# Kernel tuning notes

Hardware: AMD Instinct MI355X
Metric: run time of the kernel (lower is better)

Reference implementation:

```python
import jax, jax.numpy as jnp
import numpy as np

HID = 768
NUM_HEADS = 12
HEAD_DIM = HID // NUM_HEADS
MASK_VALUE = -1.0e9
EPS = 1.0e-4  # module's self.eps, also used as the diagonal fill constant


def setup_inputs() -> dict:
    key = jax.random.key(0)
    k1, k2, k3 = jax.random.split(key, 3)
    B, M = 16, 512
    ocr_features = jax.random.normal(k1, (B, M, HID), dtype=jnp.float32)
    # prior neighbor-attention from previous layer, probabilities in [0,1)
    prior = jax.random.uniform(k2, (B, 1, M, M), dtype=jnp.float32)
    Wq = jax.random.normal(k3, (HID, HID), dtype=jnp.float32) / np.sqrt(HID)
    bq = jnp.zeros((HID,), dtype=jnp.float32)
    ocr_features_mask = jnp.ones((B, M), dtype=jnp.int32)
    return {"ocr_features": ocr_features, "prior": prior, "Wq": Wq, "bq": bq,
            "ocr_features_mask": ocr_features_mask}


def reference(ocr_features, prior, Wq, bq, ocr_features_mask):
    B, M, _ = ocr_features.shape
    # Module uses q_linear for Q, K (and V, which is unused) -> Q == K.
    q = (ocr_features @ Wq + bq).reshape(B, M, NUM_HEADS, HEAD_DIM)
    q = q.transpose(0, 2, 1, 3)  # (B, H, M, D)
    # note: scaled by head_dim (not sqrt), as in the source
    scores = jnp.einsum('bhid,bhjd->bhij', q, q) / HEAD_DIM  # (B, H, M, M)

    dt = scores.dtype
    prev_word_mask = jnp.eye(M, k=1, dtype=dt)   # superdiagonal
    next_word_mask = jnp.eye(M, k=-1, dtype=dt)  # subdiagonal
    main_diag_mask = jnp.eye(M, dtype=dt)

    # neighbor mask: only prev/next word positions that are valid OCR tokens
    neibor_mask = ((prev_word_mask + next_word_mask)[None, :, :] > 0) & \
                  (ocr_features_mask[:, None, :] > 0)  # (B, M, M)
    scores = jnp.where(neibor_mask[:, None, :, :], scores, MASK_VALUE)
    neibor_attn = jax.nn.softmax(scores, axis=-1)
    # symmetrize: sqrt(a * a^T + eps)
    neibor_attn = jnp.sqrt(neibor_attn * jnp.swapaxes(neibor_attn, -1, -2) + EPS)
    neibor_attn = prior + (1.0 - prior) * neibor_attn

    # log-space cumulative product via triangular matmuls
    tri = jnp.triu(jnp.ones((M, M), dtype=dt))  # (M, M), incl. diagonal
    # keep only superdiagonal log-probs, cumulative-sum to the right via tri
    t = jnp.where(prev_word_mask > 0, jnp.log(neibor_attn + 1e-9), 0.0) @ tri
    g_attn = jnp.exp(jnp.einsum('ij,bhjk->bhik', tri, t))
    # zero out diagonal and lower triangle (tri - diag == 0 there)
    g_attn = jnp.where((tri - main_diag_mask) > 0, g_attn, 0.0)
    g_attn = g_attn + jnp.swapaxes(g_attn, -1, -2) + \
             jnp.where(main_diag_mask > 0, neibor_attn, EPS)
    return (g_attn, neibor_attn)
```

## Files before the change

### kernel.cpp

```cpp
#include <hip/hip_runtime.h>
#include <cstdint>
#include <cstddef>

#define B_   16
#define M_   512
#define HID_ 768
#define NH_  12
#define HD_  64

typedef short s16x8 __attribute__((ext_vector_type(8)));
typedef float f32x4 __attribute__((ext_vector_type(4)));
typedef unsigned short u16x8 __attribute__((ext_vector_type(8)));
typedef unsigned short u16x4 __attribute__((ext_vector_type(4)));

__device__ __forceinline__ unsigned short f2bf(float f) {
    unsigned int u = __builtin_bit_cast(unsigned int, f);
    u = u + 0x7FFFu + ((u >> 16) & 1u);
    return (unsigned short)(u >> 16);
}

__device__ __forceinline__ void gld_lds16(const void* g, void* lds) {
    __builtin_amdgcn_global_load_lds(
        (const __attribute__((address_space(1))) unsigned int*)g,
        (__attribute__((address_space(3))) unsigned int*)lds,
        16, 0, 0);
}

__launch_bounds__(256)
__global__ void prep(const float* __restrict__ X, const float* __restrict__ W,
                     unsigned short* __restrict__ Xb, unsigned short* __restrict__ Wt) {
    __shared__ float T[32][33];
    const int blk = blockIdx.x;
    const int t   = threadIdx.x;
    if (blk < 3072) {
        const size_t i = ((size_t)blk * 256 + t) * 8;
        const float4 a = *(const float4*)(X + i);
        const float4 b = *(const float4*)(X + i + 4);
        u16x8 v = { f2bf(a.x), f2bf(a.y), f2bf(a.z), f2bf(a.w),
                    f2bf(b.x), f2bf(b.y), f2bf(b.z), f2bf(b.w) };
        *(u16x8*)(Xb + i) = v;
    } else {
        const int tb = blk - 3072;
        const int n0 = (tb % 24) * 32;
        const int k0 = (tb / 24) * 32;
        #pragma unroll
        for (int p = 0; p < 4; ++p) {
            const int r = p * 8 + (t >> 5);
            const int c = t & 31;
            T[r][c] = W[(size_t)(k0 + r) * HID_ + n0 + c];
        }
        __syncthreads();
        const int nl = t >> 3;
        const int k4 = (t & 7) * 4;
        u16x4 v = { f2bf(T[k4 + 0][nl]), f2bf(T[k4 + 1][nl]),
                    f2bf(T[k4 + 2][nl]), f2bf(T[k4 + 3][nl]) };
        *(u16x4*)(Wt + (size_t)(n0 + nl) * HID_ + k0 + k4) = v;
    }
}

__launch_bounds__(256)
__global__ void gemm_qb(const unsigned short* __restrict__ Xb,
                        const unsigned short* __restrict__ Wt,
                        const float* __restrict__ bq, float* __restrict__ Q) {
    __shared__ unsigned short As[128 * 32];
    __shared__ unsigned short Bs[128 * 32];

    const int tid  = threadIdx.x;
    const int lane = tid & 63;
    const int wave = tid >> 6;
    const int wr   = (wave >> 1) * 64;
    const int wc   = (wave & 1) * 64;
    const int ln   = lane & 15;
    const int quad = lane >> 4;
    const int r0   = blockIdx.y * 128;
    const int n0   = blockIdx.x * 128;

    const int srow  = lane >> 2;
    const int skoff = (lane & 3) * 8;

    f32x4 acc[4][4] = {};

    for (int kt = 0; kt < HID_ / 32; ++kt) {
        const int k0 = kt * 32;
        #pragma unroll
        for (int c = wave * 2; c < wave * 2 + 2; ++c) {
            const unsigned short* ga = Xb + (size_t)(r0 + c * 16 + srow) * HID_ + k0 + skoff;
            gld_lds16(ga, (char*)As + c * 1024);
            const unsigned short* gb = Wt + (size_t)(n0 + c * 16 + srow) * HID_ + k0 + skoff;
            gld_lds16(gb, (char*)Bs + c * 1024);
        }
        __syncthreads();

        s16x8 af[4], bf[4];
        #pragma unroll
        for (int r = 0; r < 4; ++r)
            af[r] = *(const s16x8*)((const char*)As + (wr + r * 16 + ln) * 64 + quad * 16);
        #pragma unroll
        for (int c = 0; c < 4; ++c)
            bf[c] = *(const s16x8*)((const char*)Bs + (wc + c * 16 + ln) * 64 + quad * 16);
        #pragma unroll
        for (int r = 0; r < 4; ++r)
            #pragma unroll
            for (int c = 0; c < 4; ++c)
                acc[r][c] = __builtin_amdgcn_mfma_f32_16x16x32_bf16(af[r], bf[c], acc[r][c], 0, 0, 0);
        __syncthreads();
    }

    #pragma unroll
    for (int c = 0; c < 4; ++c) {
        const int col = n0 + wc + c * 16 + ln;
        const float bias = bq[col];
        #pragma unroll
        for (int r = 0; r < 4; ++r) {
            const int rowb = r0 + wr + r * 16 + quad * 4;
            #pragma unroll
            for (int e = 0; e < 4; ++e)
                Q[(size_t)(rowb + e) * HID_ + col] = acc[r][c][e] + bias;
        }
    }
}

__launch_bounds__(512)
__global__ void rowstats(const float* __restrict__ Q, const float* __restrict__ prior,
                         const int* __restrict__ mask,
                         float* __restrict__ na_super, float* __restrict__ na_sub,
                         float* __restrict__ Ssum) {
    const int bh = blockIdx.x;
    const int b  = bh / NH_;
    const int h  = bh - b * NH_;
    const int i  = threadIdx.x;
    const int lane = i & 63;
    const int wid  = i >> 6;

    __shared__ float sh_s[M_];
    __shared__ float sh_pp[M_];
    __shared__ float wsum[8];

    float s = 0.f;
    if (i < M_ - 1) {
        const float4* qa = (const float4*)(Q + (size_t)(b * M_ + i)     * HID_ + h * HD_);
        const float4* qb = (const float4*)(Q + (size_t)(b * M_ + i + 1) * HID_ + h * HD_);
        #pragma unroll
        for (int t = 0; t < 16; ++t) {
            float4 x = qa[t], y = qb[t];
            s += x.x * y.x + x.y * y.y + x.z * y.z + x.w * y.w;
        }
        s *= (1.f / 64.f);
    }
    sh_s[i] = s;
    __syncthreads();

    const bool vp = (i > 0)      && (mask[b * M_ + i - 1] > 0);
    const bool vn = (i < M_ - 1) && (mask[b * M_ + i + 1] > 0);
    const float sp = vp ? sh_s[i - 1] : -1e30f;
    const float sn = vn ? s : -1e30f;
    const float mx = fmaxf(sp, sn);
    const float ep = vp ? __expf(sp - mx) : 0.f;
    const float en = vn ? __expf(sn - mx) : 0.f;
    float den = ep + en;
    den = (den > 0.f) ? den : 1.f;
    const float pp = ep / den;
    const float pn = en / den;
    sh_pp[i] = pp;
    __syncthreads();

    float Lv = 0.f;
    if (i < M_ - 1) {
        const float  sym = sqrtf(pn * sh_pp[i + 1] + 1e-4f);
        const size_t pb  = (size_t)b * (M_ * M_);
        const float  prs = prior[pb + (size_t)i * M_ + (i + 1)];
        const float  prb = prior[pb + (size_t)(i + 1) * M_ + i];
        const float  nsup = prs + (1.f - prs) * sym;
        na_super[bh * M_ + i] = nsup;
        na_sub[bh * M_ + i]   = prb + (1.f - prb) * sym;
        Lv = logf(nsup + 1e-9f);
    }

    float v = Lv;
    #pragma unroll
    for (int off = 1; off < 64; off <<= 1) {
        float tt = __shfl_up(v, off, 64);
        if (lane >= off) v += tt;
    }
    if (lane == 63) wsum[wid] = v;
    __syncthreads();
    float base = 0.f;
    for (int w = 0; w < wid; ++w) base += wsum[w];
    Ssum[bh * M_ + i] = v + base - Lv;
}

__launch_bounds__(256)
__global__ void fill_out(const float* __restrict__ prior,
                         const float* __restrict__ na_super,
                         const float* __restrict__ na_sub,
                         const float* __restrict__ Ssum,
                         float* __restrict__ out) {
    const int tid = threadIdx.x;
    const int bi  = blockIdx.x;
    const int b   = bi >> 8;
    const int i   = ((bi & 255) << 1) | (tid >> 7);
    const int j0  = (tid & 127) * 4;

    const float4 pr4 = *(const float4*)(prior + (size_t)b * (M_ * M_) + (size_t)i * M_ + j0);
    const float pv[4] = {pr4.x, pr4.y, pr4.z, pr4.w};
    const float c0 = 0.00999999977f;
    const size_t half = (size_t)B_ * NH_ * M_ * M_;

    #pragma unroll 2
    for (int h = 0; h < NH_; ++h) {
        const int bh = b * NH_ + h;
        const float4 S4 = *(const float4*)(Ssum + (size_t)bh * M_ + j0);
        const float  Si = Ssum[bh * M_ + i];
        const float  nsup_i   = (i < M_ - 1) ? na_super[bh * M_ + i]   : 0.f;
        const float  nsub_im1 = (i > 0)      ? na_sub[bh * M_ + i - 1] : 0.f;
        const float sv[4] = {S4.x, S4.y, S4.z, S4.w};

        float nav[4], ggv[4];
        #pragma unroll
        for (int e = 0; e < 4; ++e) {
            const int j = j0 + e;
            float na = fmaf(pv[e], 1.f - c0, c0);
            if (j == i - 1) na = nsub_im1;
            if (j == i + 1) na = nsup_i;
            const float d = sv[e] - Si;
            float g = __expf((j > i) ? d : -d) + 1e-4f;
            if (j == i) g = na;
            nav[e] = na;
            ggv[e] = g;
        }

        const size_t off = ((size_t)(bh * M_ + i)) * M_ + j0;
        *(float4*)(out + off)        = make_float4(ggv[0], ggv[1], ggv[2], ggv[3]);
        *(float4*)(out + half + off) = make_float4(nav[0], nav[1], nav[2], nav[3]);
    }
}

extern "C" void kernel_launch(void* const* d_in, const int* in_sizes, int n_in,
                              void* d_out, int out_size, void* d_ws, size_t ws_size,
                              hipStream_t stream) {
    const float* X     = (const float*)d_in[0];
    const float* prior = (const float*)d_in[1];
    const float* Wq    = (const float*)d_in[2];
    const float* bq    = (const float*)d_in[3];
    const int*   msk   = (const int*)  d_in[4];
    float* out = (float*)d_out;

    float* Q        = (float*)d_ws;
    float* na_super = Q + (size_t)B_ * M_ * HID_;
    float* na_sub   = na_super + (size_t)B_ * NH_ * M_;
    float* Ssum     = na_sub   + (size_t)B_ * NH_ * M_;
    unsigned short* Xb = (unsigned short*)(Ssum + (size_t)B_ * NH_ * M_);
    unsigned short* Wt = Xb + (size_t)B_ * M_ * HID_;

    prep<<<3072 + 576, 256, 0, stream>>>(X, Wq, Xb, Wt);

    dim3 gg(HID_ / 128, (B_ * M_) / 128);
    gemm_qb<<<gg, 256, 0, stream>>>(Xb, Wt, bq, Q);

    rowstats<<<B_ * NH_, M_, 0, stream>>>(Q, prior, msk, na_super, na_sub, Ssum);

    fill_out<<<B_ * (M_ / 2), 256, 0, stream>>>(prior, na_super, na_sub, Ssum, out);
}
```

Measured before the change: 469.2 us.

## Widen GEMM K-tile with swizzled LDS, split dot pass, nontemporal output stores

The GEMM now loads 64-wide K tiles with an XOR-swizzled LDS layout, which halves the number of barrier pairs and is meant to avoid bank conflicts. The neighbor dot products move out of the 192-block rowstats kernel into a separate, widely parallel wave-per-row kernel with shuffle reductions, so the scan kernel only reads precomputed dots. The fill kernel uses nontemporal loads and stores for prior and the large output to reduce cache pollution. This adds one extra kernel launch and reuses the Xb workspace buffer for the dot results.

```diff
diff --git a/kernel.cpp b/kernel.cpp
--- a/kernel.cpp
+++ b/kernel.cpp
@@ -62,8 +62,8 @@
 __global__ void gemm_qb(const unsigned short* __restrict__ Xb,
                         const unsigned short* __restrict__ Wt,
                         const float* __restrict__ bq, float* __restrict__ Q) {
-    __shared__ unsigned short As[128 * 32];
-    __shared__ unsigned short Bs[128 * 32];
+    __shared__ unsigned short As[128 * 64];
+    __shared__ unsigned short Bs[128 * 64];
 
     const int tid  = threadIdx.x;
     const int lane = tid & 63;
@@ -75,34 +75,40 @@
     const int r0   = blockIdx.y * 128;
     const int n0   = blockIdx.x * 128;
 
-    const int srow  = lane >> 2;
-    const int skoff = (lane & 3) * 8;
+    const int srow  = lane >> 3;
+    const int selem = ((lane & 7) ^ (lane >> 3)) * 8;
+    const int swz   = (ln & 7) << 4;
 
     f32x4 acc[4][4] = {};
 
-    for (int kt = 0; kt < HID_ / 32; ++kt) {
-        const int k0 = kt * 32;
-        #pragma unroll
-        for (int c = wave * 2; c < wave * 2 + 2; ++c) {
-            const unsigned short* ga = Xb + (size_t)(r0 + c * 16 + srow) * HID_ + k0 + skoff;
+    for (int kt = 0; kt < HID_ / 64; ++kt) {
+        const int k0 = kt * 64;
+        #pragma unroll
+        for (int c = wave * 4; c < wave * 4 + 4; ++c) {
+            const unsigned short* ga = Xb + (size_t)(r0 + c * 8 + srow) * HID_ + k0 + selem;
             gld_lds16(ga, (char*)As + c * 1024);
-            const unsigned short* gb = Wt + (size_t)(n0 + c * 16 + srow) * HID_ + k0 + skoff;
+            const unsigned short* gb = Wt + (size_t)(n0 + c * 8 + srow) * HID_ + k0 + selem;
             gld_lds16(gb, (char*)Bs + c * 1024);
         }
         __syncthreads();
 
-        s16x8 af[4], bf[4];
-        #pragma unroll
-        for (int r = 0; r < 4; ++r)
-            af[r] = *(const s16x8*)((const char*)As + (wr + r * 16 + ln) * 64 + quad * 16);
-        #pragma unroll
-        for (int c = 0; c < 4; ++c)
-            bf[c] = *(const s16x8*)((const char*)Bs + (wc + c * 16 + ln) * 64 + quad * 16);
-        #pragma unroll
-        for (int r = 0; r < 4; ++r)
+        #pragma unroll
+        for (int kk = 0; kk < 2; ++kk) {
+            s16x8 af[4], bf[4];
+            #pragma unroll
+            for (int r = 0; r < 4; ++r)
+                af[r] = *(const s16x8*)((const char*)As + (wr + r * 16 + ln) * 128
+                                        + ((kk * 64 + quad * 16) ^ swz));
             #pragma unroll
             for (int c = 0; c < 4; ++c)
-                acc[r][c] = __builtin_amdgcn_mfma_f32_16x16x32_bf16(af[r], bf[c], acc[r][c], 0, 0, 0);
+                bf[c] = *(const s16x8*)((const char*)Bs + (wc + c * 16 + ln) * 128
+                                        + ((kk * 64 + quad * 16) ^ swz));
+            #pragma unroll
+            for (int r = 0; r < 4; ++r)
+                #pragma unroll
+                for (int c = 0; c < 4; ++c)
+                    acc[r][c] = __builtin_amdgcn_mfma_f32_16x16x32_bf16(af[r], bf[c], acc[r][c], 0, 0, 0);
+        }
         __syncthreads();
     }
 
@@ -120,14 +126,40 @@
     }
 }
 
+__launch_bounds__(256)
+__global__ void dots(const float* __restrict__ Q, float* __restrict__ sdot) {
+    const int w    = blockIdx.x * 4 + (threadIdx.x >> 6);
+    const int lane = threadIdx.x & 63;
+    const int b    = w >> 9;
+    const int i    = w & 511;
+    if (i >= M_ - 1) return;
+
+    const float* ra = Q + (size_t)(b * M_ + i) * HID_;
+    const float* rb = ra + HID_;
+
+    #pragma unroll
+    for (int c = 0; c < 3; ++c) {
+        const int e = c * 256 + lane * 4;
+        const float4 a = *(const float4*)(ra + e);
+        const float4 bq4 = *(const float4*)(rb + e);
+        float p = a.x * bq4.x + a.y * bq4.y + a.z * bq4.z + a.w * bq4.w;
+        #pragma unroll
+        for (int off = 1; off < 16; off <<= 1)
+            p += __shfl_xor(p, off, 64);
+        if ((lane & 15) == 0) {
+            const int h = c * 4 + (lane >> 4);
+            sdot[(size_t)(b * NH_ + h) * M_ + i] = p * (1.f / 64.f);
+        }
+    }
+}
+
 __launch_bounds__(512)
-__global__ void rowstats(const float* __restrict__ Q, const float* __restrict__ prior,
-                         const int* __restrict__ mask,
-                         float* __restrict__ na_super, float* __restrict__ na_sub,
-                         float* __restrict__ Ssum) {
+__global__ void scanstats(const float* __restrict__ sdot, const float* __restrict__ prior,
+                          const int* __restrict__ mask,
+                          float* __restrict__ na_super, float* __restrict__ na_sub,
+                          float* __restrict__ Ssum) {
     const int bh = blockIdx.x;
     const int b  = bh / NH_;
-    const int h  = bh - b * NH_;
     const int i  = threadIdx.x;
     const int lane = i & 63;
     const int wid  = i >> 6;
@@ -136,17 +168,7 @@
     __shared__ float sh_pp[M_];
     __shared__ float wsum[8];
 
-    float s = 0.f;
-    if (i < M_ - 1) {
-        const float4* qa = (const float4*)(Q + (size_t)(b * M_ + i)     * HID_ + h * HD_);
-        const float4* qb = (const float4*)(Q + (size_t)(b * M_ + i + 1) * HID_ + h * HD_);
-        #pragma unroll
-        for (int t = 0; t < 16; ++t) {
-            float4 x = qa[t], y = qb[t];
-            s += x.x * y.x + x.y * y.y + x.z * y.z + x.w * y.w;
-        }
-        s *= (1.f / 64.f);
-    }
+    const float s = (i < M_ - 1) ? sdot[bh * M_ + i] : 0.f;
     sh_s[i] = s;
     __syncthreads();
 
@@ -201,8 +223,9 @@
     const int i   = ((bi & 255) << 1) | (tid >> 7);
     const int j0  = (tid & 127) * 4;
 
-    const float4 pr4 = *(const float4*)(prior + (size_t)b * (M_ * M_) + (size_t)i * M_ + j0);
-    const float pv[4] = {pr4.x, pr4.y, pr4.z, pr4.w};
+    const f32x4 pr4 = __builtin_nontemporal_load(
+        (const f32x4*)(prior + (size_t)b * (M_ * M_) + (size_t)i * M_ + j0));
+    const float pv[4] = {pr4[0], pr4[1], pr4[2], pr4[3]};
     const float c0 = 0.00999999977f;
     const size_t half = (size_t)B_ * NH_ * M_ * M_;
 
@@ -215,7 +238,7 @@
         const float  nsub_im1 = (i > 0)      ? na_sub[bh * M_ + i - 1] : 0.f;
         const float sv[4] = {S4.x, S4.y, S4.z, S4.w};
 
-        float nav[4], ggv[4];
+        f32x4 nav, ggv;
         #pragma unroll
         for (int e = 0; e < 4; ++e) {
             const int j = j0 + e;
@@ -230,8 +253,8 @@
         }
 
         const size_t off = ((size_t)(bh * M_ + i)) * M_ + j0;
-        *(float4*)(out + off)        = make_float4(ggv[0], ggv[1], ggv[2], ggv[3]);
-        *(float4*)(out + half + off) = make_float4(nav[0], nav[1], nav[2], nav[3]);
+        __builtin_nontemporal_store(ggv, (f32x4*)(out + off));
+        __builtin_nontemporal_store(nav, (f32x4*)(out + half + off));
     }
 }
 
@@ -251,13 +274,16 @@
     float* Ssum     = na_sub   + (size_t)B_ * NH_ * M_;
     unsigned short* Xb = (unsigned short*)(Ssum + (size_t)B_ * NH_ * M_);
     unsigned short* Wt = Xb + (size_t)B_ * M_ * HID_;
+    float* sdot     = (float*)Xb;
 
     prep<<<3072 + 576, 256, 0, stream>>>(X, Wq, Xb, Wt);
 
     dim3 gg(HID_ / 128, (B_ * M_) / 128);
     gemm_qb<<<gg, 256, 0, stream>>>(Xb, Wt, bq, Q);
 
-    rowstats<<<B_ * NH_, M_, 0, stream>>>(Q, prior, msk, na_super, na_sub, Ssum);
+    dots<<<2048, 256, 0, stream>>>(Q, sdot);
+
+    scanstats<<<B_ * NH_, M_, 0, stream>>>(sdot, prior, msk, na_super, na_sub, Ssum);
 
     fill_out<<<B_ * (M_ / 2), 256, 0, stream>>>(prior, na_super, na_sub, Ssum, out);
 }
```

New measurement: 462.9 us. No clear change (-1.4%).
